# Performance work log

Measured on AMD Instinct MI355X. Metric: run time of the kernel, lower is better.

Reference implementation:

```python
import jax, jax.numpy as jnp
import numpy as np
import math

N = 100000        # nodes
E = 3200000       # edges (avg degree 32)
DIN = 128         # in_features
DOUT = 64         # out_features
LAMDA = 0.5       # GCNII lambda
ALPHA = 0.1       # GCNII alpha
L = 1             # layer index


def setup_inputs() -> dict:
    key = jax.random.key(0)
    ks = jax.random.split(key, 6)
    x = jax.random.normal(ks[0], (N, DIN), dtype=jnp.float32)
    adj_rows = jnp.sort(jax.random.randint(ks[1], (E,), 0, N, dtype=jnp.int32))
    adj_cols = jax.random.randint(ks[2], (E,), 0, N, dtype=jnp.int32)
    adj_vals = jax.random.uniform(ks[3], (E,), dtype=jnp.float32)
    h0 = jax.random.normal(ks[4], (N, DOUT), dtype=jnp.float32)
    weight = jax.random.normal(ks[5], (DIN, DOUT), dtype=jnp.float32) * 0.02  # xavier-ish gain 0.02
    bias = jnp.zeros((1, DOUT), dtype=jnp.float32)
    return {"x": x, "adj_rows": adj_rows, "adj_cols": adj_cols,
            "adj_vals": adj_vals, "h0": h0, "weight": weight, "bias": bias}


def reference(x, adj_rows, adj_cols, adj_vals, h0, weight, bias):
    theta = math.log(LAMDA / L + 1)
    # dense projection: [N, DIN] @ [DIN, DOUT]
    xw = x @ weight
    # SpMM: hi[r] = sum_{e: rows[e]==r} vals[e] * xw[cols[e]]
    hi = jax.ops.segment_sum(adj_vals[:, None] * xw[adj_cols], adj_rows, num_segments=N)
    # non-variant GCNII combine
    support = (1.0 - ALPHA) * hi + ALPHA * h0
    r = support
    out = theta * support + (1.0 - theta) * r
    return out + bias
```

## Files before the change

### kernel.cpp

```cpp
#include <hip/hip_runtime.h>

#define N_NODES 100000
#define N_EDGES 3200000
#define DIN     128
#define DOUT    64
#define GEMM_BLOCKS 1563
#define RP_BLOCKS   12500

typedef unsigned short bf16_t;
typedef float f32x4  __attribute__((ext_vector_type(4)));
typedef short bf16x8 __attribute__((ext_vector_type(8)));

__device__ __forceinline__ bf16_t f32_to_bf16(float f) {
    union { float f; unsigned int u; } un; un.f = f;
    unsigned int u = un.u + 0x7fffu + ((un.u >> 16) & 1u);
    return (bf16_t)(u >> 16);
}
__device__ __forceinline__ unsigned int pack2(float lo, float hi) {
    return (unsigned int)f32_to_bf16(lo) | ((unsigned int)f32_to_bf16(hi) << 16);
}
__device__ __forceinline__ float2 bf16x2_to_f32x2(unsigned int p) {
    union { unsigned int u; float f; } lo, hi;
    lo.u = p << 16;
    hi.u = p & 0xffff0000u;
    return make_float2(lo.f, hi.f);
}

#define UNPACK_FMA(ACC, G, VV)                                    \
    do {                                                          \
        const float2 _f0 = bf16x2_to_f32x2((G).x);                \
        const float2 _f1 = bf16x2_to_f32x2((G).y);                \
        const float2 _f2 = bf16x2_to_f32x2((G).z);                \
        const float2 _f3 = bf16x2_to_f32x2((G).w);                \
        ACC[0] += (VV) * _f0.x; ACC[1] += (VV) * _f0.y;           \
        ACC[2] += (VV) * _f1.x; ACC[3] += (VV) * _f1.y;           \
        ACC[4] += (VV) * _f2.x; ACC[5] += (VV) * _f2.y;           \
        ACC[6] += (VV) * _f3.x; ACC[7] += (VV) * _f3.y;           \
    } while (0)

#define MASKED_GROUP(ACC, EBASE, END)                                       \
    do {                                                                    \
        const int   _ei = (EBASE) + grp;                                    \
        const bool  _ok = _ei < (END);                                      \
        const int   _ec = _ok ? _ei : ((END) - 1);                          \
        const int   _cc = cols[_ec];                                        \
        const float _vv = _ok ? vals[_ec] : 0.f;                            \
        const uint4 _g  = *(const uint4*)&xwb[(size_t)_cc * DOUT + 8 * fq]; \
        UNPACK_FMA(ACC, _g, _vv);                                           \
    } while (0)

#define OCTET4(ACC, P)                                                      \
    do {                                                                    \
        const int   _c0 = cols[(P) + grp];                                  \
        const int   _c1 = cols[(P) + 8  + grp];                             \
        const int   _c2 = cols[(P) + 16 + grp];                             \
        const int   _c3 = cols[(P) + 24 + grp];                             \
        const float _v0 = vals[(P) + grp];                                  \
        const float _v1 = vals[(P) + 8  + grp];                             \
        const float _v2 = vals[(P) + 16 + grp];                             \
        const float _v3 = vals[(P) + 24 + grp];                             \
        const uint4 _g0 = *(const uint4*)&xwb[(size_t)_c0 * DOUT + 8 * fq]; \
        const uint4 _g1 = *(const uint4*)&xwb[(size_t)_c1 * DOUT + 8 * fq]; \
        const uint4 _g2 = *(const uint4*)&xwb[(size_t)_c2 * DOUT + 8 * fq]; \
        const uint4 _g3 = *(const uint4*)&xwb[(size_t)_c3 * DOUT + 8 * fq]; \
        UNPACK_FMA(ACC, _g0, _v0);                                          \
        UNPACK_FMA(ACC, _g1, _v1);                                          \
        UNPACK_FMA(ACC, _g2, _v2);                                          \
        UNPACK_FMA(ACC, _g3, _v3);                                          \
    } while (0)

__global__ __launch_bounds__(256) void gemm_rowptr(const float* __restrict__ x,
                                                   const float* __restrict__ w,
                                                   const int*   __restrict__ rows,
                                                   bf16_t* __restrict__ xwb,
                                                   int* __restrict__ row_ptr) {
    __shared__ unsigned short Xs[64][DIN];
    __shared__ unsigned short Wt[DOUT][DIN];

    const int bid = blockIdx.x;
    const int tid = threadIdx.x;

    if (bid >= GEMM_BLOCKS) {
        const int e = (bid - GEMM_BLOCKS) * 256 + tid;
        if (e < N_EDGES) {
            const int cur  = rows[e];
            const int prev = (e == 0) ? -1 : rows[e - 1];
            for (int r = prev + 1; r <= cur; ++r) row_ptr[r] = e;
            if (e == N_EDGES - 1)
                for (int r = cur + 1; r <= N_NODES; ++r) row_ptr[r] = N_EDGES;
        }
        return;
    }

    const int block_row = bid * 64;

    {
        const float4* w4 = (const float4*)w;
#pragma unroll
        for (int i = 0; i < 8; ++i) {
            const int f4 = i * 256 + tid;
            const float4 v = w4[f4];
            const int base = f4 * 4;
            const int k = base >> 6;
            const int n = base & 63;
            Wt[n + 0][(((k >> 3) ^ ((n + 0) & 7)) << 3) | (k & 7)] = f32_to_bf16(v.x);
            Wt[n + 1][(((k >> 3) ^ ((n + 1) & 7)) << 3) | (k & 7)] = f32_to_bf16(v.y);
            Wt[n + 2][(((k >> 3) ^ ((n + 2) & 7)) << 3) | (k & 7)] = f32_to_bf16(v.z);
            Wt[n + 3][(((k >> 3) ^ ((n + 3) & 7)) << 3) | (k & 7)] = f32_to_bf16(v.w);
        }
    }
    {
        const int r = tid >> 2;
        const int q = tid & 3;
        const int gr = block_row + r;
        const float4* xp = (const float4*)&x[(size_t)gr * DIN + q * 32];
        const bool ok = gr < N_NODES;
#pragma unroll
        for (int ci = 0; ci < 4; ++ci) {
            float4 a = make_float4(0.f, 0.f, 0.f, 0.f), b = a;
            if (ok) { a = xp[2 * ci]; b = xp[2 * ci + 1]; }
            uint4 pk;
            pk.x = pack2(a.x, a.y);
            pk.y = pack2(a.z, a.w);
            pk.z = pack2(b.x, b.y);
            pk.w = pack2(b.z, b.w);
            const int c = q * 4 + ci;
            *(uint4*)&Xs[r][(c ^ (r & 7)) << 3] = pk;
        }
    }
    __syncthreads();

    const int wv_ = tid >> 6;
    const int l   = tid & 63;
    const int lr  = l & 15;
    const int hi  = l >> 4;
    const int arow = wv_ * 16 + lr;

    f32x4 acc0 = {0.f, 0.f, 0.f, 0.f};
    f32x4 acc1 = acc0, acc2 = acc0, acc3 = acc0;
#pragma unroll
    for (int s = 0; s < 4; ++s) {
        const int kc = s * 4 + hi;
        const bf16x8 a  = *(const bf16x8*)&Xs[arow][(kc ^ (arow & 7)) << 3];
        const int bc = (kc ^ (lr & 7)) << 3;
        const bf16x8 b0 = *(const bf16x8*)&Wt[lr     ][bc];
        const bf16x8 b1 = *(const bf16x8*)&Wt[16 + lr][bc];
        const bf16x8 b2 = *(const bf16x8*)&Wt[32 + lr][bc];
        const bf16x8 b3 = *(const bf16x8*)&Wt[48 + lr][bc];
        acc0 = __builtin_amdgcn_mfma_f32_16x16x32_bf16(a, b0, acc0, 0, 0, 0);
        acc1 = __builtin_amdgcn_mfma_f32_16x16x32_bf16(a, b1, acc1, 0, 0, 0);
        acc2 = __builtin_amdgcn_mfma_f32_16x16x32_bf16(a, b2, acc2, 0, 0, 0);
        acc3 = __builtin_amdgcn_mfma_f32_16x16x32_bf16(a, b3, acc3, 0, 0, 0);
    }

#pragma unroll
    for (int reg = 0; reg < 4; ++reg) {
        const int grow = block_row + wv_ * 16 + hi * 4 + reg;
        if (grow < N_NODES) {
            bf16_t* o = &xwb[(size_t)grow * DOUT + lr];
            o[0]  = f32_to_bf16(acc0[reg]);
            o[16] = f32_to_bf16(acc1[reg]);
            o[32] = f32_to_bf16(acc2[reg]);
            o[48] = f32_to_bf16(acc3[reg]);
        }
    }
}

__global__ __launch_bounds__(256) void spmm2(const bf16_t* __restrict__ xwb,
                                             const int*    __restrict__ row_ptr,
                                             const int*    __restrict__ cols,
                                             const float*  __restrict__ vals,
                                             const float*  __restrict__ h0,
                                             const float*  __restrict__ bias,
                                             float* __restrict__ out) {
    const int wid  = (blockIdx.x * blockDim.x + threadIdx.x) >> 6;
    const int lane = threadIdx.x & 63;
    const int r0 = wid << 1;
    if (r0 >= N_NODES) return;

    const int grp = lane >> 3;
    const int fq  = lane & 7;
    const bool has1 = (r0 + 1) < N_NODES;

    const int s0 = __builtin_amdgcn_readfirstlane(row_ptr[r0]);
    const int m0 = __builtin_amdgcn_readfirstlane(row_ptr[r0 + 1]);
    const int e1 = has1 ? __builtin_amdgcn_readfirstlane(row_ptr[r0 + 2]) : m0;

    const int rsel = (grp == 1 && has1) ? (r0 + 1) : r0;
    const f32x4 ha = __builtin_nontemporal_load((const f32x4*)&h0[(size_t)rsel * DOUT + 8 * fq]);
    const f32x4 hb = __builtin_nontemporal_load((const f32x4*)&h0[(size_t)rsel * DOUT + 8 * fq + 4]);
    const f32x4 ba = *(const f32x4*)&bias[8 * fq];
    const f32x4 bb = *(const f32x4*)&bias[8 * fq + 4];

    float accA[8] = {};
    float accB[8] = {};
    int p0 = s0, p1 = m0;

    while (p0 + 16 <= m0 && p1 + 16 <= e1) {
        const int   c00 = cols[p0 + grp];
        const int   c01 = cols[p0 + 8 + grp];
        const int   c10 = cols[p1 + grp];
        const int   c11 = cols[p1 + 8 + grp];
        const float v00 = vals[p0 + grp];
        const float v01 = vals[p0 + 8 + grp];
        const float v10 = vals[p1 + grp];
        const float v11 = vals[p1 + 8 + grp];
        const uint4 g00 = *(const uint4*)&xwb[(size_t)c00 * DOUT + 8 * fq];
        const uint4 g01 = *(const uint4*)&xwb[(size_t)c01 * DOUT + 8 * fq];
        const uint4 g10 = *(const uint4*)&xwb[(size_t)c10 * DOUT + 8 * fq];
        const uint4 g11 = *(const uint4*)&xwb[(size_t)c11 * DOUT + 8 * fq];
        UNPACK_FMA(accA, g00, v00);
        UNPACK_FMA(accA, g01, v01);
        UNPACK_FMA(accB, g10, v10);
        UNPACK_FMA(accB, g11, v11);
        p0 += 16; p1 += 16;
    }
    for (; p0 + 32 <= m0; p0 += 32) OCTET4(accA, p0);
    for (; p0 < m0; p0 += 16) {
        MASKED_GROUP(accA, p0, m0);
        if (p0 + 8 < m0) MASKED_GROUP(accA, p0 + 8, m0);
    }
    for (; p1 + 32 <= e1; p1 += 32) OCTET4(accB, p1);
    for (; p1 < e1; p1 += 16) {
        MASKED_GROUP(accB, p1, e1);
        if (p1 + 8 < e1) MASKED_GROUP(accB, p1 + 8, e1);
    }

#define RED(ACC, J, S)                                   \
    do {                                                 \
        float _t = ACC[J];                               \
        _t += __shfl_xor(_t, 8, 64);                     \
        _t += __shfl_xor(_t, 16, 64);                    \
        _t += __shfl_xor(_t, 32, 64);                    \
        S = _t;                                          \
    } while (0)
    float a0, a1, a2, a3, a4, a5, a6, a7;
    float b0, b1, b2, b3, b4, b5, b6, b7;
    RED(accA, 0, a0); RED(accA, 1, a1); RED(accA, 2, a2); RED(accA, 3, a3);
    RED(accA, 4, a4); RED(accA, 5, a5); RED(accA, 6, a6); RED(accA, 7, a7);
    RED(accB, 0, b0); RED(accB, 1, b1); RED(accB, 2, b2); RED(accB, 3, b3);
    RED(accB, 4, b4); RED(accB, 5, b5); RED(accB, 6, b6); RED(accB, 7, b7);
#undef RED

    if (grp == 0 || (grp == 1 && has1)) {
        const bool g1 = (grp == 1);
        const float t0 = g1 ? b0 : a0;
        const float t1 = g1 ? b1 : a1;
        const float t2 = g1 ? b2 : a2;
        const float t3 = g1 ? b3 : a3;
        const float t4 = g1 ? b4 : a4;
        const float t5 = g1 ? b5 : a5;
        const float t6 = g1 ? b6 : a6;
        const float t7 = g1 ? b7 : a7;
        f32x4 ra, rb;
        ra.x = 0.9f * t0 + 0.1f * ha.x + ba.x;
        ra.y = 0.9f * t1 + 0.1f * ha.y + ba.y;
        ra.z = 0.9f * t2 + 0.1f * ha.z + ba.z;
        ra.w = 0.9f * t3 + 0.1f * ha.w + ba.w;
        rb.x = 0.9f * t4 + 0.1f * hb.x + bb.x;
        rb.y = 0.9f * t5 + 0.1f * hb.y + bb.y;
        rb.z = 0.9f * t6 + 0.1f * hb.z + bb.z;
        rb.w = 0.9f * t7 + 0.1f * hb.w + bb.w;
        __builtin_nontemporal_store(ra, (f32x4*)&out[(size_t)rsel * DOUT + 8 * fq]);
        __builtin_nontemporal_store(rb, (f32x4*)&out[(size_t)rsel * DOUT + 8 * fq + 4]);
    }
}

extern "C" void kernel_launch(void* const* d_in, const int* in_sizes, int n_in,
                              void* d_out, int out_size, void* d_ws, size_t ws_size,
                              hipStream_t stream) {
    const float* x    = (const float*)d_in[0];
    const int*   rows = (const int*)  d_in[1];
    const int*   cols = (const int*)  d_in[2];
    const float* vals = (const float*)d_in[3];
    const float* h0   = (const float*)d_in[4];
    const float* w    = (const float*)d_in[5];
    const float* bias = (const float*)d_in[6];
    float* out = (float*)d_out;

    bf16_t* xwb = (bf16_t*)d_ws;
    const size_t xw_bytes = (size_t)N_NODES * DOUT * sizeof(bf16_t);
    int* row_ptr = (int*)((char*)d_ws + xw_bytes);

    gemm_rowptr<<<GEMM_BLOCKS + RP_BLOCKS, 256, 0, stream>>>(x, w, rows, xwb, row_ptr);
    spmm2<<<(N_NODES / 2 * 64 + 255) / 256, 256, 0, stream>>>(
        xwb, row_ptr, cols, vals, h0, bias, out);
}
```

Measured before the change: 97.66 us.

## Split projected features into two column halves and gather each half separately

The GEMM now writes xw as two separate column-half planes of 32 bf16 features each. The SpMM is rewritten so that each wavefront handles one row and one half, processing 16 edges in parallel with 4 lanes per edge. Because the whole first half-plane is gathered before the second, each pass touches a 6.4MB table that fits more easily in cache, which should raise the L2/MALL hit rate for random gathers. The trade-off is twice as many wavefronts, with cols, vals and row_ptr read twice and an extra shuffle step in the reduction.

Result: slower. 117.7 us (+20.5%).

```diff
diff --git a/kernel.cpp b/kernel.cpp
--- a/kernel.cpp
+++ b/kernel.cpp
@@ -38,35 +38,15 @@
         ACC[6] += (VV) * _f3.x; ACC[7] += (VV) * _f3.y;           \
     } while (0)
 
-#define MASKED_GROUP(ACC, EBASE, END)                                       \
-    do {                                                                    \
-        const int   _ei = (EBASE) + grp;                                    \
-        const bool  _ok = _ei < (END);                                      \
-        const int   _ec = _ok ? _ei : ((END) - 1);                          \
-        const int   _cc = cols[_ec];                                        \
-        const float _vv = _ok ? vals[_ec] : 0.f;                            \
-        const uint4 _g  = *(const uint4*)&xwb[(size_t)_cc * DOUT + 8 * fq]; \
-        UNPACK_FMA(ACC, _g, _vv);                                           \
-    } while (0)
-
-#define OCTET4(ACC, P)                                                      \
-    do {                                                                    \
-        const int   _c0 = cols[(P) + grp];                                  \
-        const int   _c1 = cols[(P) + 8  + grp];                             \
-        const int   _c2 = cols[(P) + 16 + grp];                             \
-        const int   _c3 = cols[(P) + 24 + grp];                             \
-        const float _v0 = vals[(P) + grp];                                  \
-        const float _v1 = vals[(P) + 8  + grp];                             \
-        const float _v2 = vals[(P) + 16 + grp];                             \
-        const float _v3 = vals[(P) + 24 + grp];                             \
-        const uint4 _g0 = *(const uint4*)&xwb[(size_t)_c0 * DOUT + 8 * fq]; \
-        const uint4 _g1 = *(const uint4*)&xwb[(size_t)_c1 * DOUT + 8 * fq]; \
-        const uint4 _g2 = *(const uint4*)&xwb[(size_t)_c2 * DOUT + 8 * fq]; \
-        const uint4 _g3 = *(const uint4*)&xwb[(size_t)_c3 * DOUT + 8 * fq]; \
-        UNPACK_FMA(ACC, _g0, _v0);                                          \
-        UNPACK_FMA(ACC, _g1, _v1);                                          \
-        UNPACK_FMA(ACC, _g2, _v2);                                          \
-        UNPACK_FMA(ACC, _g3, _v3);                                          \
+#define MASKED_GROUP16(ACC, EBASE)                                      \
+    do {                                                                \
+        const int   _ei = (EBASE) + grp;                                \
+        const bool  _ok = _ei < end;                                    \
+        const int   _ec = _ok ? _ei : (end - 1);                        \
+        const int   _cc = cols[_ec];                                    \
+        const float _vv = _ok ? vals[_ec] : 0.f;                        \
+        const uint4 _g  = *(const uint4*)&xh[(size_t)_cc * 32 + 8 * fq];\
+        UNPACK_FMA(ACC, _g, _vv);                                       \
     } while (0)
 
 __global__ __launch_bounds__(256) void gemm_rowptr(const float* __restrict__ x,
@@ -157,112 +137,88 @@
     for (int reg = 0; reg < 4; ++reg) {
         const int grow = block_row + wv_ * 16 + hi * 4 + reg;
         if (grow < N_NODES) {
-            bf16_t* o = &xwb[(size_t)grow * DOUT + lr];
-            o[0]  = f32_to_bf16(acc0[reg]);
-            o[16] = f32_to_bf16(acc1[reg]);
-            o[32] = f32_to_bf16(acc2[reg]);
-            o[48] = f32_to_bf16(acc3[reg]);
-        }
-    }
-}
-
-__global__ __launch_bounds__(256) void spmm2(const bf16_t* __restrict__ xwb,
-                                             const int*    __restrict__ row_ptr,
-                                             const int*    __restrict__ cols,
-                                             const float*  __restrict__ vals,
-                                             const float*  __restrict__ h0,
-                                             const float*  __restrict__ bias,
-                                             float* __restrict__ out) {
+            bf16_t* o0 = &xwb[(size_t)grow * 32 + lr];
+            bf16_t* o1 = &xwb[(size_t)N_NODES * 32 + (size_t)grow * 32 + lr];
+            o0[0]  = f32_to_bf16(acc0[reg]);
+            o0[16] = f32_to_bf16(acc1[reg]);
+            o1[0]  = f32_to_bf16(acc2[reg]);
+            o1[16] = f32_to_bf16(acc3[reg]);
+        }
+    }
+}
+
+__global__ __launch_bounds__(256) void spmm_half(const bf16_t* __restrict__ xwb,
+                                                 const int*    __restrict__ row_ptr,
+                                                 const int*    __restrict__ cols,
+                                                 const float*  __restrict__ vals,
+                                                 const float*  __restrict__ h0,
+                                                 const float*  __restrict__ bias,
+                                                 float* __restrict__ out) {
     const int wid  = (blockIdx.x * blockDim.x + threadIdx.x) >> 6;
     const int lane = threadIdx.x & 63;
-    const int r0 = wid << 1;
-    if (r0 >= N_NODES) return;
-
-    const int grp = lane >> 3;
-    const int fq  = lane & 7;
-    const bool has1 = (r0 + 1) < N_NODES;
-
-    const int s0 = __builtin_amdgcn_readfirstlane(row_ptr[r0]);
-    const int m0 = __builtin_amdgcn_readfirstlane(row_ptr[r0 + 1]);
-    const int e1 = has1 ? __builtin_amdgcn_readfirstlane(row_ptr[r0 + 2]) : m0;
-
-    const int rsel = (grp == 1 && has1) ? (r0 + 1) : r0;
-    const f32x4 ha = __builtin_nontemporal_load((const f32x4*)&h0[(size_t)rsel * DOUT + 8 * fq]);
-    const f32x4 hb = __builtin_nontemporal_load((const f32x4*)&h0[(size_t)rsel * DOUT + 8 * fq + 4]);
-    const f32x4 ba = *(const f32x4*)&bias[8 * fq];
-    const f32x4 bb = *(const f32x4*)&bias[8 * fq + 4];
+    if (wid >= 2 * N_NODES) return;
+
+    const int half = (wid >= N_NODES) ? 1 : 0;
+    const int row  = __builtin_amdgcn_readfirstlane(wid - half * N_NODES);
+
+    const int grp = lane >> 2;
+    const int fq  = lane & 3;
+
+    const bf16_t* xh = xwb + (size_t)half * N_NODES * 32;
+    const int fbase = half * 32 + 8 * fq;
+
+    const int start = __builtin_amdgcn_readfirstlane(row_ptr[row]);
+    const int end   = __builtin_amdgcn_readfirstlane(row_ptr[row + 1]);
+
+    const f32x4 ha = __builtin_nontemporal_load((const f32x4*)&h0[(size_t)row * DOUT + fbase]);
+    const f32x4 hb = __builtin_nontemporal_load((const f32x4*)&h0[(size_t)row * DOUT + fbase + 4]);
+    const f32x4 ba = *(const f32x4*)&bias[fbase];
+    const f32x4 bb = *(const f32x4*)&bias[fbase + 4];
 
     float accA[8] = {};
     float accB[8] = {};
-    int p0 = s0, p1 = m0;
-
-    while (p0 + 16 <= m0 && p1 + 16 <= e1) {
-        const int   c00 = cols[p0 + grp];
-        const int   c01 = cols[p0 + 8 + grp];
-        const int   c10 = cols[p1 + grp];
-        const int   c11 = cols[p1 + 8 + grp];
-        const float v00 = vals[p0 + grp];
-        const float v01 = vals[p0 + 8 + grp];
-        const float v10 = vals[p1 + grp];
-        const float v11 = vals[p1 + 8 + grp];
-        const uint4 g00 = *(const uint4*)&xwb[(size_t)c00 * DOUT + 8 * fq];
-        const uint4 g01 = *(const uint4*)&xwb[(size_t)c01 * DOUT + 8 * fq];
-        const uint4 g10 = *(const uint4*)&xwb[(size_t)c10 * DOUT + 8 * fq];
-        const uint4 g11 = *(const uint4*)&xwb[(size_t)c11 * DOUT + 8 * fq];
-        UNPACK_FMA(accA, g00, v00);
-        UNPACK_FMA(accA, g01, v01);
-        UNPACK_FMA(accB, g10, v10);
-        UNPACK_FMA(accB, g11, v11);
-        p0 += 16; p1 += 16;
-    }
-    for (; p0 + 32 <= m0; p0 += 32) OCTET4(accA, p0);
-    for (; p0 < m0; p0 += 16) {
-        MASKED_GROUP(accA, p0, m0);
-        if (p0 + 8 < m0) MASKED_GROUP(accA, p0 + 8, m0);
-    }
-    for (; p1 + 32 <= e1; p1 += 32) OCTET4(accB, p1);
-    for (; p1 < e1; p1 += 16) {
-        MASKED_GROUP(accB, p1, e1);
-        if (p1 + 8 < e1) MASKED_GROUP(accB, p1 + 8, e1);
-    }
-
-#define RED(ACC, J, S)                                   \
+    int e = start;
+
+    for (; e + 32 <= end; e += 32) {
+        const int   c0 = cols[e + grp];
+        const int   c1 = cols[e + 16 + grp];
+        const float v0 = vals[e + grp];
+        const float v1 = vals[e + 16 + grp];
+        const uint4 g0 = *(const uint4*)&xh[(size_t)c0 * 32 + 8 * fq];
+        const uint4 g1 = *(const uint4*)&xh[(size_t)c1 * 32 + 8 * fq];
+        UNPACK_FMA(accA, g0, v0);
+        UNPACK_FMA(accB, g1, v1);
+    }
+    for (; e < end; e += 16) {
+        MASKED_GROUP16(accA, e);
+    }
+
+    float s0, s1, s2, s3, s4, s5, s6, s7;
+#define RED(SJ, J)                                       \
     do {                                                 \
-        float _t = ACC[J];                               \
+        float _t = accA[J] + accB[J];                    \
+        _t += __shfl_xor(_t, 4, 64);                     \
         _t += __shfl_xor(_t, 8, 64);                     \
         _t += __shfl_xor(_t, 16, 64);                    \
         _t += __shfl_xor(_t, 32, 64);                    \
-        S = _t;                                          \
+        SJ = _t;                                         \
     } while (0)
-    float a0, a1, a2, a3, a4, a5, a6, a7;
-    float b0, b1, b2, b3, b4, b5, b6, b7;
-    RED(accA, 0, a0); RED(accA, 1, a1); RED(accA, 2, a2); RED(accA, 3, a3);
-    RED(accA, 4, a4); RED(accA, 5, a5); RED(accA, 6, a6); RED(accA, 7, a7);
-    RED(accB, 0, b0); RED(accB, 1, b1); RED(accB, 2, b2); RED(accB, 3, b3);
-    RED(accB, 4, b4); RED(accB, 5, b5); RED(accB, 6, b6); RED(accB, 7, b7);
+    RED(s0, 0); RED(s1, 1); RED(s2, 2); RED(s3, 3);
+    RED(s4, 4); RED(s5, 5); RED(s6, 6); RED(s7, 7);
 #undef RED
 
-    if (grp == 0 || (grp == 1 && has1)) {
-        const bool g1 = (grp == 1);
-        const float t0 = g1 ? b0 : a0;
-        const float t1 = g1 ? b1 : a1;
-        const float t2 = g1 ? b2 : a2;
-        const float t3 = g1 ? b3 : a3;
-        const float t4 = g1 ? b4 : a4;
-        const float t5 = g1 ? b5 : a5;
-        const float t6 = g1 ? b6 : a6;
-        const float t7 = g1 ? b7 : a7;
+    if (grp == 0) {
         f32x4 ra, rb;
-        ra.x = 0.9f * t0 + 0.1f * ha.x + ba.x;
-        ra.y = 0.9f * t1 + 0.1f * ha.y + ba.y;
-        ra.z = 0.9f * t2 + 0.1f * ha.z + ba.z;
-        ra.w = 0.9f * t3 + 0.1f * ha.w + ba.w;
-        rb.x = 0.9f * t4 + 0.1f * hb.x + bb.x;
-        rb.y = 0.9f * t5 + 0.1f * hb.y + bb.y;
-        rb.z = 0.9f * t6 + 0.1f * hb.z + bb.z;
-        rb.w = 0.9f * t7 + 0.1f * hb.w + bb.w;
-        __builtin_nontemporal_store(ra, (f32x4*)&out[(size_t)rsel * DOUT + 8 * fq]);
-        __builtin_nontemporal_store(rb, (f32x4*)&out[(size_t)rsel * DOUT + 8 * fq + 4]);
+        ra.x = 0.9f * s0 + 0.1f * ha.x + ba.x;
+        ra.y = 0.9f * s1 + 0.1f * ha.y + ba.y;
+        ra.z = 0.9f * s2 + 0.1f * ha.z + ba.z;
+        ra.w = 0.9f * s3 + 0.1f * ha.w + ba.w;
+        rb.x = 0.9f * s4 + 0.1f * hb.x + bb.x;
+        rb.y = 0.9f * s5 + 0.1f * hb.y + bb.y;
+        rb.z = 0.9f * s6 + 0.1f * hb.z + bb.z;
+        rb.w = 0.9f * s7 + 0.1f * hb.w + bb.w;
+        __builtin_nontemporal_store(ra, (f32x4*)&out[(size_t)row * DOUT + fbase]);
+        __builtin_nontemporal_store(rb, (f32x4*)&out[(size_t)row * DOUT + fbase + 4]);
     }
 }
 
@@ -283,6 +239,6 @@
     int* row_ptr = (int*)((char*)d_ws + xw_bytes);
 
     gemm_rowptr<<<GEMM_BLOCKS + RP_BLOCKS, 256, 0, stream>>>(x, w, rows, xwb, row_ptr);
-    spmm2<<<(N_NODES / 2 * 64 + 255) / 256, 256, 0, stream>>>(
+    spmm_half<<<(2 * N_NODES + 3) / 4, 256, 0, stream>>>(
         xwb, row_ptr, cols, vals, h0, bias, out);
 }
```
